# Kernel optimization log

Hardware: AMD Instinct MI355X
Metric: run time of the kernel (lower is better)

## Reference

```python
import jax, jax.numpy as jnp
import numpy as np

HIDDEN = 1024
INTER = 1408
N_EXPERTS = 8
TOP_K = 2
BATCH, SEQ = 2, 1024


def setup_inputs() -> dict:
    key = jax.random.key(0)
    k1, k2, k3, k4, k5 = jax.random.split(key, 5)
    scale_in = 1.0 / np.sqrt(HIDDEN)
    scale_mid = 1.0 / np.sqrt(INTER)
    return {
        "hidden_states": jax.random.normal(k1, (BATCH, SEQ, HIDDEN), dtype=jnp.float32),
        # router: torch Linear(hidden, n_experts, bias=False) -> weight [E, hidden]
        "router_w": jax.random.normal(k2, (N_EXPERTS, HIDDEN), dtype=jnp.float32) * scale_in,
        # per-expert SwiGLU MLP weights, stored pre-transposed for x @ W
        "wg": jax.random.normal(k3, (N_EXPERTS, HIDDEN, INTER), dtype=jnp.float32) * scale_in,
        "wu": jax.random.normal(k4, (N_EXPERTS, HIDDEN, INTER), dtype=jnp.float32) * scale_in,
        "wd": jax.random.normal(k5, (N_EXPERTS, INTER, HIDDEN), dtype=jnp.float32) * scale_mid,
    }


def reference(hidden_states, router_w, wg, wu, wd):
    B, S, D = hidden_states.shape
    x = hidden_states.reshape(-1, D)  # [T, D]
    T = x.shape[0]
    E = router_w.shape[0]

    # Router: softmax over experts in float32, then top-k and renormalize (norm_topk_prob=True)
    logits = x @ router_w.T  # [T, E]
    probs = jax.nn.softmax(logits.astype(jnp.float32), axis=-1)
    topk_w, topk_idx = jax.lax.top_k(probs, TOP_K)  # [T, K]
    topk_w = topk_w / jnp.sum(topk_w, axis=-1, keepdims=True)
    topk_w = topk_w.astype(x.dtype)

    # Dense combine weights [T, E]: zero for unrouted experts -> math-identical to sparse dispatch
    combine = jnp.zeros((T, E), dtype=x.dtype).at[
        jnp.arange(T)[:, None], topk_idx
    ].add(topk_w)

    # Expert SwiGLU MLPs computed as batched GEMMs over experts
    g = jnp.einsum('td,edf->etf', x, wg)  # [E, T, INTER]
    u = jnp.einsum('td,edf->etf', x, wu)
    h = jax.nn.silu(g) * u
    y = jnp.einsum('etf,efd->etd', h, wd)  # [E, T, D]

    out = jnp.einsum('etd,te->td', y, combine)  # weighted combine
    return out.reshape(B, S, D)
```

## Files before the change

kernel.cpp:

```cpp
#include <hip/hip_runtime.h>
#include <math.h>

#define HIDDEN 1024
#define INTER  1408
#define NEXP   8
#define NTOK   2048
#define KSPLIT_LEN 704

typedef short s16x8 __attribute__((ext_vector_type(8)));
typedef float f32x4 __attribute__((ext_vector_type(4)));

static __device__ __forceinline__ short f2b(float f) {
  union { float f; unsigned u; } v; v.f = f;
  unsigned u = v.u;
  unsigned r = (u + 0x7FFFu + ((u >> 16) & 1u)) >> 16;
  return (short)r;
}

__global__ __launch_bounds__(256) void router_choice(
    const float* __restrict__ x, const float* __restrict__ rw,
    int* __restrict__ ce, float2* __restrict__ cw)
{
  int wave = threadIdx.x >> 6;
  int lane = threadIdx.x & 63;
  int t = blockIdx.x * 4 + wave;
  if (t >= NTOK) return;
  const float* xt = x + (size_t)t * HIDDEN;
  float xr[16];
#pragma unroll
  for (int i = 0; i < 16; ++i) xr[i] = xt[lane + 64 * i];
  float logits[NEXP];
#pragma unroll
  for (int e = 0; e < NEXP; ++e) {
    const float* w = rw + e * HIDDEN;
    float acc = 0.f;
#pragma unroll
    for (int i = 0; i < 16; ++i) acc = fmaf(xr[i], w[lane + 64 * i], acc);
#pragma unroll
    for (int off = 32; off > 0; off >>= 1) acc += __shfl_xor(acc, off);
    logits[e] = acc;
  }
  if (lane == 0) {
    float mx = logits[0];
#pragma unroll
    for (int e = 1; e < NEXP; ++e) mx = fmaxf(mx, logits[e]);
    float p[NEXP];
#pragma unroll
    for (int e = 0; e < NEXP; ++e) p[e] = expf(logits[e] - mx);
    int i0 = 0;
#pragma unroll
    for (int e = 1; e < NEXP; ++e) if (p[e] > p[i0]) i0 = e;
    int i1 = (i0 == 0) ? 1 : 0;
#pragma unroll
    for (int e = 0; e < NEXP; ++e) { if (e != i0 && p[e] > p[i1]) i1 = e; }
    float denom = p[i0] + p[i1];
    ce[t] = i0 | (i1 << 8);
    cw[t] = make_float2(p[i0] / denom, p[i1] / denom);
  }
}

__global__ __launch_bounds__(256) void build_lists(
    const int* __restrict__ ce, const float2* __restrict__ cw,
    int* __restrict__ counts, int* __restrict__ base,
    int* __restrict__ tok_list, float* __restrict__ w_list)
{
  int e = blockIdx.x;
  int tid = threadIdx.x;
  __shared__ int hall[256][8];
  __shared__ int hsum[8];
  __shared__ int scan[256];

  int cloc[8];
  int h[8] = {0,0,0,0,0,0,0,0};
  int myc = 0;
#pragma unroll
  for (int j = 0; j < 8; ++j) {
    int c = ce[tid * 8 + j];
    cloc[j] = c;
    int e0 = c & 255, e1 = (c >> 8) & 255;
    h[e0]++; h[e1]++;
    myc += (e0 == e) + (e1 == e);
  }
#pragma unroll
  for (int k = 0; k < 8; ++k) hall[tid][k] = h[k];
  scan[tid] = myc;
  __syncthreads();

  if (tid < 8) {
    int s = 0;
    for (int i = 0; i < 256; ++i) s += hall[i][tid];
    hsum[tid] = s;
  }
  int v = myc;
  for (int off = 1; off < 256; off <<= 1) {
    int prev = (tid >= off) ? scan[tid - off] : 0;
    __syncthreads();
    v = v + prev;
    scan[tid] = v;
    __syncthreads();
  }
  int pos = v - myc;

  if (tid == 0) {
    int b = 0;
    for (int k = 0; k < e; ++k) b += hsum[k];
    base[e] = b;
    counts[e] = hsum[e];
  }

#pragma unroll
  for (int j = 0; j < 8; ++j) {
    int t = tid * 8 + j;
    int c = cloc[j];
    int e0 = c & 255, e1 = (c >> 8) & 255;
    if (e0 == e) {
      float2 w = cw[t];
      tok_list[e * NTOK + pos] = t;
      w_list[e * NTOK + pos] = w.x;
      pos++;
    } else if (e1 == e) {
      float2 w = cw[t];
      tok_list[e * NTOK + pos] = t | (1 << 16);
      w_list[e * NTOK + pos] = w.y;
      pos++;
    }
  }
}

static __device__ __forceinline__ void tconv_tile(
    const float* __restrict__ ie, short* __restrict__ oe,
    int K, int N, int k0, int n0, int tid, float (*t)[65])
{
  int c4 = (tid & 15) * 4, r = tid >> 4;
#pragma unroll
  for (int p = 0; p < 4; ++p) {
    float4 v = *(const float4*)(ie + (size_t)(k0 + r + p * 16) * N + n0 + c4);
    t[r + p * 16][c4 + 0] = v.x;
    t[r + p * 16][c4 + 1] = v.y;
    t[r + p * 16][c4 + 2] = v.z;
    t[r + p * 16][c4 + 3] = v.w;
  }
  __syncthreads();
  int rn = tid >> 2, ck = (tid & 3) * 16;
  s16x8 o0, o1;
#pragma unroll
  for (int j = 0; j < 8; ++j) o0[j] = f2b(t[ck + j][rn]);
#pragma unroll
  for (int j = 0; j < 8; ++j) o1[j] = f2b(t[ck + 8 + j][rn]);
  short* op = oe + (size_t)(n0 + rn) * K + k0 + ck;
  *(s16x8*)(op) = o0;
  *(s16x8*)(op + 8) = o1;
}

__global__ __launch_bounds__(256) void prep_kernel(
    const float* __restrict__ x, const float* __restrict__ wg,
    const float* __restrict__ wu, const float* __restrict__ wd,
    short* __restrict__ xb, short* __restrict__ wgT,
    short* __restrict__ wuT, short* __restrict__ wdT)
{
  __shared__ float t[64][65];
  int id = blockIdx.x;
  int tid = threadIdx.x;
  if (id < 1024) {
    size_t i = (size_t)id * 256 + tid;
    const float4* p = (const float4*)x;
    float4 a = p[2 * i], b = p[2 * i + 1];
    s16x8 o;
    o[0] = f2b(a.x); o[1] = f2b(a.y); o[2] = f2b(a.z); o[3] = f2b(a.w);
    o[4] = f2b(b.x); o[5] = f2b(b.y); o[6] = f2b(b.z); o[7] = f2b(b.w);
    *(s16x8*)(xb + 8 * i) = o;
    return;
  }
  int id2 = id - 1024;
  int seg = id2 / 2816;
  int r = id2 - seg * 2816;
  int e = r / 352;
  int rem = r - e * 352;
  if (seg < 2) {
    int kt = rem / 22, nt = rem - kt * 22;
    const float* ie = (seg == 0 ? wg : wu) + (size_t)e * HIDDEN * INTER;
    short* oe = (seg == 0 ? wgT : wuT) + (size_t)e * HIDDEN * INTER;
    tconv_tile(ie, oe, HIDDEN, INTER, kt * 64, nt * 64, tid, t);
  } else {
    int kt = rem >> 4, nt = rem & 15;
    const float* ie = wd + (size_t)e * HIDDEN * INTER;
    short* oe = wdT + (size_t)e * HIDDEN * INTER;
    tconv_tile(ie, oe, INTER, HIDDEN, kt * 64, nt * 64, tid, t);
  }
}


__global__ __launch_bounds__(256, 2) void gateup_mfma(
    const short* __restrict__ xb, const short* __restrict__ wgT,
    const short* __restrict__ wuT,
    const int* __restrict__ counts, const int* __restrict__ base,
    const int* __restrict__ tok_list, short* __restrict__ hbuf)
{
  int id = blockIdx.x;
  int xcd = id & 7;
  int rest = id >> 3;
  int mslot = rest & 15;
  int g = (rest >> 4) * 8 + xcd;
  int e = g / 11;
  int n0 = (g - e * 11) * 128;
  int cnt = counts[e];
  int m0 = mslot * 128;
  if (m0 >= cnt) return;

  __shared__ short As[128 * 32];
  __shared__ short Bg[128 * 32];
  __shared__ short Bu[128 * 32];
  __shared__ int toks[128];

  int tid = threadIdx.x;
  if (tid < 128) {
    int r = m0 + tid;
    toks[tid] = tok_list[e * NTOK + (r < cnt ? r : cnt - 1)] & 0xFFFF;
  }
  __syncthreads();

  int sr = tid >> 1;
  int h = tid & 1;
  int key = (sr >> 1) & 3;
  int pair = ((2 * h) ^ key) >> 1;
  int sw = (key & 1) * 8;
  const short* gA = xb + (size_t)toks[sr] * HIDDEN + pair * 16;
  const short* gG = wgT + ((size_t)e * INTER + n0 + sr) * HIDDEN + pair * 16;
  const short* gU = wuT + ((size_t)e * INTER + n0 + sr) * HIDDEN + pair * 16;
  short* wA0 = &As[sr * 32 + h * 16 + sw];
  short* wA1 = &As[sr * 32 + h * 16 + (8 - sw)];
  short* wG0 = &Bg[sr * 32 + h * 16 + sw];
  short* wG1 = &Bg[sr * 32 + h * 16 + (8 - sw)];
  short* wU0 = &Bu[sr * 32 + h * 16 + sw];
  short* wU1 = &Bu[sr * 32 + h * 16 + (8 - sw)];

  int wv = tid >> 6, lane = tid & 63;
  int wm = wv & 1, wn = wv >> 1;
  int q = lane >> 4, ml = lane & 15;
  int chk = q ^ ((ml >> 1) & 3);
  const short* ard = &As[(wm * 64 + ml) * 32 + chk * 8];
  const short* grd = &Bg[(wn * 64 + ml) * 32 + chk * 8];
  const short* urd = &Bu[(wn * 64 + ml) * 32 + chk * 8];

  f32x4 accg[4][4], accu[4][4];
#pragma unroll
  for (int i = 0; i < 4; ++i)
#pragma unroll
    for (int j = 0; j < 4; ++j) { accg[i][j] = (f32x4)0.f; accu[i][j] = (f32x4)0.f; }

  s16x8 a0 = *(const s16x8*)(gA);     s16x8 a1 = *(const s16x8*)(gA + 8);
  s16x8 g0 = *(const s16x8*)(gG);     s16x8 g1 = *(const s16x8*)(gG + 8);
  s16x8 u0 = *(const s16x8*)(gU);     s16x8 u1 = *(const s16x8*)(gU + 8);

  for (int k0 = 0; k0 < HIDDEN; k0 += 32) {
    __syncthreads();
    *(s16x8*)wA0 = a0; *(s16x8*)wA1 = a1;
    *(s16x8*)wG0 = g0; *(s16x8*)wG1 = g1;
    *(s16x8*)wU0 = u0; *(s16x8*)wU1 = u1;
    __syncthreads();

    int kn = (k0 + 32) & (HIDDEN - 1);
    a0 = *(const s16x8*)(gA + kn);     a1 = *(const s16x8*)(gA + kn + 8);
    g0 = *(const s16x8*)(gG + kn);     g1 = *(const s16x8*)(gG + kn + 8);
    u0 = *(const s16x8*)(gU + kn);     u1 = *(const s16x8*)(gU + kn + 8);

    s16x8 af[4], gf[4], uf[4];
#pragma unroll
    for (int i = 0; i < 4; ++i) af[i] = *(const s16x8*)(ard + i * 16 * 32);
#pragma unroll
    for (int j = 0; j < 4; ++j) {
      gf[j] = *(const s16x8*)(grd + j * 16 * 32);
      uf[j] = *(const s16x8*)(urd + j * 16 * 32);
    }
#pragma unroll
    for (int i = 0; i < 4; ++i)
#pragma unroll
      for (int j = 0; j < 4; ++j) {
        accg[i][j] = __builtin_amdgcn_mfma_f32_16x16x32_bf16(af[i], gf[j], accg[i][j], 0, 0, 0);
        accu[i][j] = __builtin_amdgcn_mfma_f32_16x16x32_bf16(af[i], uf[j], accu[i][j], 0, 0, 0);
      }
  }

  int hb = base[e];
#pragma unroll
  for (int i = 0; i < 4; ++i)
#pragma unroll
    for (int ii = 0; ii < 4; ++ii) {
      int r = m0 + wm * 64 + i * 16 + q * 4 + ii;
      if (r < cnt) {
        short* hp = hbuf + (size_t)(hb + r) * INTER + n0 + wn * 64 + ml;
#pragma unroll
        for (int j = 0; j < 4; ++j) {
          float gg = accg[i][j][ii], uu = accu[i][j][ii];
          float hh = (gg / (1.f + __expf(-gg))) * uu;
          hp[j * 16] = f2b(hh);
        }
      }
    }
}

__global__ __launch_bounds__(256, 3) void down_mfma(
    const short* __restrict__ hbuf, const short* __restrict__ wdT,
    const int* __restrict__ counts, const int* __restrict__ base,
    const int* __restrict__ tok_list, const float* __restrict__ w_list,
    float* __restrict__ ybuf)
{
  int id = blockIdx.x;
  int xcd = id & 7;
  int rest = id >> 3;
  int mslot = rest & 15;
  int g = (rest >> 4) * 8 + xcd;
  int e = g >> 4;
  int ks = (g >> 3) & 1;
  int n0 = (g & 7) * 128;
  int cnt = counts[e];
  int m0 = mslot * 128;
  if (m0 >= cnt) return;

  __shared__ short As[128 * 32];
  __shared__ short Bs[128 * 32];

  int tid = threadIdx.x;
  int hb = base[e];
  int kbeg = ks * KSPLIT_LEN, kend = kbeg + KSPLIT_LEN;

  int sr = tid >> 1;
  int h = tid & 1;
  int key = (sr >> 1) & 3;
  int pair = ((2 * h) ^ key) >> 1;
  int sw = (key & 1) * 8;
  int ra = m0 + sr; if (ra >= cnt) ra = cnt - 1;
  const short* gA = hbuf + (size_t)(hb + ra) * INTER + pair * 16;
  const short* gB = wdT + ((size_t)e * HIDDEN + n0 + sr) * INTER + pair * 16;
  short* wA0 = &As[sr * 32 + h * 16 + sw];
  short* wA1 = &As[sr * 32 + h * 16 + (8 - sw)];
  short* wB0 = &Bs[sr * 32 + h * 16 + sw];
  short* wB1 = &Bs[sr * 32 + h * 16 + (8 - sw)];

  int wv = tid >> 6, lane = tid & 63;
  int wm = wv & 1, wn = wv >> 1;
  int q = lane >> 4, ml = lane & 15;
  int chk = q ^ ((ml >> 1) & 3);
  const short* ard = &As[(wm * 64 + ml) * 32 + chk * 8];
  const short* brd = &Bs[(wn * 64 + ml) * 32 + chk * 8];

  f32x4 acc[4][4];
#pragma unroll
  for (int i = 0; i < 4; ++i)
#pragma unroll
    for (int j = 0; j < 4; ++j) acc[i][j] = (f32x4)0.f;

  s16x8 a0 = *(const s16x8*)(gA + kbeg);  s16x8 a1 = *(const s16x8*)(gA + kbeg + 8);
  s16x8 b0 = *(const s16x8*)(gB + kbeg);  s16x8 b1 = *(const s16x8*)(gB + kbeg + 8);

  for (int k0 = kbeg; k0 < kend; k0 += 32) {
    __syncthreads();
    *(s16x8*)wA0 = a0; *(s16x8*)wA1 = a1;
    *(s16x8*)wB0 = b0; *(s16x8*)wB1 = b1;
    __syncthreads();

    int kn = k0 + 32; if (kn >= kend) kn = kbeg;
    a0 = *(const s16x8*)(gA + kn);  a1 = *(const s16x8*)(gA + kn + 8);
    b0 = *(const s16x8*)(gB + kn);  b1 = *(const s16x8*)(gB + kn + 8);

    s16x8 af[4], bf[4];
#pragma unroll
    for (int i = 0; i < 4; ++i) af[i] = *(const s16x8*)(ard + i * 16 * 32);
#pragma unroll
    for (int j = 0; j < 4; ++j) bf[j] = *(const s16x8*)(brd + j * 16 * 32);
#pragma unroll
    for (int i = 0; i < 4; ++i)
#pragma unroll
      for (int j = 0; j < 4; ++j)
        acc[i][j] = __builtin_amdgcn_mfma_f32_16x16x32_bf16(af[i], bf[j], acc[i][j], 0, 0, 0);
  }

#pragma unroll
  for (int i = 0; i < 4; ++i)
#pragma unroll
    for (int ii = 0; ii < 4; ++ii) {
      int r = m0 + wm * 64 + i * 16 + q * 4 + ii;
      if (r < cnt) {
        int ent = tok_list[e * NTOK + r];
        int tok = ent & 0xFFFF, slot = ent >> 16;
        float wgt = w_list[e * NTOK + r];
        float* yp = ybuf + ((size_t)(slot * 2 + ks) * NTOK + tok) * HIDDEN
                    + n0 + wn * 64 + ml;
#pragma unroll
        for (int j = 0; j < 4; ++j)
          yp[j * 16] = acc[i][j][ii] * wgt;
      }
    }
}

__global__ __launch_bounds__(256) void combine_kernel(
    const float* __restrict__ ybuf, float* __restrict__ out)
{
  size_t i = (size_t)blockIdx.x * 256 + threadIdx.x;
  const size_t S = (size_t)NTOK * HIDDEN / 4;
  float4 a = ((const float4*)ybuf)[i];
  float4 b = ((const float4*)ybuf)[i + S];
  float4 c = ((const float4*)ybuf)[i + 2 * S];
  float4 d = ((const float4*)ybuf)[i + 3 * S];
  float4 o;
  o.x = (a.x + b.x) + (c.x + d.x);
  o.y = (a.y + b.y) + (c.y + d.y);
  o.z = (a.z + b.z) + (c.z + d.z);
  o.w = (a.w + b.w) + (c.w + d.w);
  ((float4*)out)[i] = o;
}

extern "C" void kernel_launch(void* const* d_in, const int* in_sizes, int n_in,
                              void* d_out, int out_size, void* d_ws, size_t ws_size,
                              hipStream_t stream)
{
  const float* x  = (const float*)d_in[0];
  const float* rw = (const float*)d_in[1];
  const float* wg = (const float*)d_in[2];
  const float* wu = (const float*)d_in[3];
  const float* wd = (const float*)d_in[4];
  float* out = (float*)d_out;

  char* ws = (char*)d_ws;
  int*    counts   = (int*)(ws);
  int*    base     = (int*)(ws + 32);
  int*    tok_list = (int*)(ws + 64);
  float*  w_list   = (float*)(ws + 64 + NEXP * NTOK * 4);
  size_t off = 64 + 2 * (size_t)NEXP * NTOK * 4;
  int*    ce = (int*)(ws + off);     off += NTOK * 4;
  float2* cw = (float2*)(ws + off);  off += NTOK * 8;
  short* xb  = (short*)(ws + off);  off += (size_t)NTOK * HIDDEN * 2;
  short* wgT = (short*)(ws + off);  off += (size_t)NEXP * HIDDEN * INTER * 2;
  short* wuT = (short*)(ws + off);  off += (size_t)NEXP * HIDDEN * INTER * 2;
  short* wdT = (short*)(ws + off);  off += (size_t)NEXP * HIDDEN * INTER * 2;
  short* hbuf = (short*)(ws + off);
  float* ybuf = (float*)wgT;

  router_choice<<<NTOK / 4, 256, 0, stream>>>(x, rw, ce, cw);
  build_lists<<<NEXP, 256, 0, stream>>>(ce, cw, counts, base, tok_list, w_list);

  prep_kernel<<<1024 + 3 * 2816, 256, 0, stream>>>(x, wg, wu, wd, xb, wgT, wuT, wdT);

  gateup_mfma<<<8 * 16 * 11, 256, 0, stream>>>(xb, wgT, wuT, counts, base, tok_list, hbuf);
  down_mfma<<<8 * 16 * 16, 256, 0, stream>>>(hbuf, wdT, counts, base, tok_list, w_list, ybuf);

  combine_kernel<<<(NTOK * HIDDEN / 4) / 256, 256, 0, stream>>>(ybuf, out);
}
```

Before: 277.6 us.

## Fuse x bf16 conversion into router and rewrite weight transpose without LDS

```diff
diff --git a/kernel.cpp b/kernel.cpp
--- a/kernel.cpp
+++ b/kernel.cpp
@@ -19,7 +19,7 @@
 
 __global__ __launch_bounds__(256) void router_choice(
     const float* __restrict__ x, const float* __restrict__ rw,
-    int* __restrict__ ce, float2* __restrict__ cw)
+    int* __restrict__ ce, float2* __restrict__ cw, short* __restrict__ xb)
 {
   int wave = threadIdx.x >> 6;
   int lane = threadIdx.x & 63;
@@ -29,6 +29,11 @@
   float xr[16];
 #pragma unroll
   for (int i = 0; i < 16; ++i) xr[i] = xt[lane + 64 * i];
+
+  short* xo = xb + (size_t)t * HIDDEN;
+#pragma unroll
+  for (int i = 0; i < 16; ++i) xo[lane + 64 * i] = f2b(xr[i]);
+
   float logits[NEXP];
 #pragma unroll
   for (int e = 0; e < NEXP; ++e) {
@@ -127,65 +132,50 @@
   }
 }
 
-static __device__ __forceinline__ void tconv_tile(
-    const float* __restrict__ ie, short* __restrict__ oe,
-    int K, int N, int k0, int n0, int tid, float (*t)[65])
-{
-  int c4 = (tid & 15) * 4, r = tid >> 4;
-#pragma unroll
-  for (int p = 0; p < 4; ++p) {
-    float4 v = *(const float4*)(ie + (size_t)(k0 + r + p * 16) * N + n0 + c4);
-    t[r + p * 16][c4 + 0] = v.x;
-    t[r + p * 16][c4 + 1] = v.y;
-    t[r + p * 16][c4 + 2] = v.z;
-    t[r + p * 16][c4 + 3] = v.w;
-  }
-  __syncthreads();
-  int rn = tid >> 2, ck = (tid & 3) * 16;
-  s16x8 o0, o1;
-#pragma unroll
-  for (int j = 0; j < 8; ++j) o0[j] = f2b(t[ck + j][rn]);
-#pragma unroll
-  for (int j = 0; j < 8; ++j) o1[j] = f2b(t[ck + 8 + j][rn]);
-  short* op = oe + (size_t)(n0 + rn) * K + k0 + ck;
-  *(s16x8*)(op) = o0;
-  *(s16x8*)(op + 8) = o1;
-}
-
-__global__ __launch_bounds__(256) void prep_kernel(
-    const float* __restrict__ x, const float* __restrict__ wg,
-    const float* __restrict__ wu, const float* __restrict__ wd,
-    short* __restrict__ xb, short* __restrict__ wgT,
-    short* __restrict__ wuT, short* __restrict__ wdT)
-{
-  __shared__ float t[64][65];
+__global__ __launch_bounds__(256) void wconv(
+    const float* __restrict__ wg, const float* __restrict__ wu,
+    const float* __restrict__ wd,
+    short* __restrict__ wgT, short* __restrict__ wuT, short* __restrict__ wdT)
+{
   int id = blockIdx.x;
-  int tid = threadIdx.x;
-  if (id < 1024) {
-    size_t i = (size_t)id * 256 + tid;
-    const float4* p = (const float4*)x;
-    float4 a = p[2 * i], b = p[2 * i + 1];
-    s16x8 o;
-    o[0] = f2b(a.x); o[1] = f2b(a.y); o[2] = f2b(a.z); o[3] = f2b(a.w);
-    o[4] = f2b(b.x); o[5] = f2b(b.y); o[6] = f2b(b.z); o[7] = f2b(b.w);
-    *(s16x8*)(xb + 8 * i) = o;
-    return;
-  }
-  int id2 = id - 1024;
-  int seg = id2 / 2816;
-  int r = id2 - seg * 2816;
-  int e = r / 352;
-  int rem = r - e * 352;
-  if (seg < 2) {
-    int kt = rem / 22, nt = rem - kt * 22;
-    const float* ie = (seg == 0 ? wg : wu) + (size_t)e * HIDDEN * INTER;
-    short* oe = (seg == 0 ? wgT : wuT) + (size_t)e * HIDDEN * INTER;
-    tconv_tile(ie, oe, HIDDEN, INTER, kt * 64, nt * 64, tid, t);
-  } else {
-    int kt = rem >> 4, nt = rem & 15;
-    const float* ie = wd + (size_t)e * HIDDEN * INTER;
-    short* oe = wdT + (size_t)e * HIDDEN * INTER;
-    tconv_tile(ie, oe, INTER, HIDDEN, kt * 64, nt * 64, tid, t);
+  int wave = threadIdx.x >> 6;
+  int lane = threadIdx.x & 63;
+  int mat = id / 1408;
+  int r = id - mat * 1408;
+  int e = r / 176;
+  int t = r - e * 176;
+
+  const float* src; short* dst; int K, N;
+  if (mat == 0)      { src = wg; dst = wgT; K = HIDDEN; N = INTER; }
+  else if (mat == 1) { src = wu; dst = wuT; K = HIDDEN; N = INTER; }
+  else               { src = wd; dst = wdT; K = INTER;  N = HIDDEN; }
+
+  int nstr = N >> 6;
+  int ks = t / nstr, nt = t - ks * nstr;
+  int n0 = nt * 64;
+  int k0 = ks * 128 + wave * 32;
+
+  const float* se = src + (size_t)e * (HIDDEN * INTER);
+  short*       de = dst + (size_t)e * (HIDDEN * INTER);
+  int n = n0 + lane;
+
+  float v[32];
+#pragma unroll
+  for (int j = 0; j < 32; ++j) v[j] = se[(size_t)(k0 + j) * N + n];
+
+  unsigned pk[16];
+#pragma unroll
+  for (int j = 0; j < 16; ++j) {
+    unsigned lo = (unsigned short)f2b(v[2 * j]);
+    unsigned hi = (unsigned short)f2b(v[2 * j + 1]);
+    pk[j] = lo | (hi << 16);
+  }
+
+  short* dp = de + (size_t)n * K + k0;
+#pragma unroll
+  for (int c = 0; c < 4; ++c) {
+    uint4 o = make_uint4(pk[4 * c], pk[4 * c + 1], pk[4 * c + 2], pk[4 * c + 3]);
+    *(uint4*)(dp + 8 * c) = o;
   }
 }
 
@@ -436,10 +426,10 @@
   short* hbuf = (short*)(ws + off);
   float* ybuf = (float*)wgT;
 
-  router_choice<<<NTOK / 4, 256, 0, stream>>>(x, rw, ce, cw);
+  router_choice<<<NTOK / 4, 256, 0, stream>>>(x, rw, ce, cw, xb);
   build_lists<<<NEXP, 256, 0, stream>>>(ce, cw, counts, base, tok_list, w_list);
 
-  prep_kernel<<<1024 + 3 * 2816, 256, 0, stream>>>(x, wg, wu, wd, xb, wgT, wuT, wdT);
+  wconv<<<3 * NEXP * 176, 256, 0, stream>>>(wg, wu, wd, wgT, wuT, wdT);
 
   gateup_mfma<<<8 * 16 * 11, 256, 0, stream>>>(xb, wgT, wuT, counts, base, tok_list, hbuf);
   down_mfma<<<8 * 16 * 16, 256, 0, stream>>>(hbuf, wdT, counts, base, tok_list, w_list, ybuf);
```

Measured after the change: 287.4 us. 3.5% more time.
